# Kernel optimization log

Measured on AMD Instinct MI355X. Metric: run time of the kernel, lower is better.

The kernel has to match this reference:

```python
import jax, jax.numpy as jnp
import numpy as np

B, LV, HW, LT, D, H = 4, 16, 196, 32, 768, 12
DH = D // H
SCALE = 1.0 / np.sqrt(DH).astype(np.float32)


def _lin(x, W, b):
    # torch nn.Linear convention: W is [out, in]
    return x @ W.T + b


def _split_heads(x):
    # (..., D) -> (..., H, DH)
    return x.reshape(*x.shape[:-1], H, DH)


def _attn_logits(feat_q, feat_k, mask_q, mask_k, Wq, bq, Wk, bk):
    # feat_q: (B, LV, Lq, D), feat_k: (B, LV, Lk, D)
    q = _split_heads(_lin(feat_q, Wq, bq))  # b v q h d
    k = _split_heads(_lin(feat_k, Wk, bk))  # b v k h d
    logits = jnp.einsum('bvqhd,bvkhd->bvhqk', q, k)
    m = (mask_q[:, :, None] & mask_k[:, None, :])[:, None, None]  # b 1 1 q k
    return jnp.where(m, logits, -10000.0)


def setup_inputs() -> dict:
    key = jax.random.key(0)
    ks = jax.random.split(key, 12)
    inp = {
        'vid_feat': jax.random.normal(ks[0], (B, LV, HW, D), jnp.float32),
        'txt_feat': jax.random.normal(ks[1], (B, LV, LT, D), jnp.float32),
        'vid_mask': jnp.ones((B, LV), dtype=bool),
        'txt_mask': jax.random.randint(ks[2], (B, LT), 0, 2) > 0,
    }
    for i, name in enumerate(['v2v', 't2v', 't2t', 'v2t']):
        inp[name + '_W'] = jax.random.normal(ks[3 + 2 * i], (3, D, D), jnp.float32) * 0.02
        inp[name + '_b'] = jnp.zeros((3, D), jnp.float32)
    return inp


def reference(vid_feat, txt_feat, vid_mask, txt_mask,
              v2v_W, v2v_b, t2v_W, t2v_b, t2t_W, t2t_b, v2t_W, v2t_b):
    mask_hw = jnp.ones((vid_feat.shape[0], HW), dtype=bool)

    # values: concat video-keys then text-keys along the key axis
    v_value = jnp.concatenate([_lin(vid_feat, v2v_W[2], v2v_b[2]),
                               _lin(txt_feat, t2v_W[2], t2v_b[2])], axis=2)
    v_value = _split_heads(v_value)  # b v (HW+LT) h d
    t_value = jnp.concatenate([_lin(vid_feat, v2t_W[2], v2t_b[2]),
                               _lin(txt_feat, t2t_W[2], t2t_b[2])], axis=2)
    t_value = _split_heads(t_value)

    # logits (source call order: get_attn_logits(feat_k, mask_k, feat_q, mask_q, ...))
    v2v = _attn_logits(vid_feat, vid_feat, mask_hw, mask_hw, v2v_W[0], v2v_b[0], v2v_W[1], v2v_b[1])
    t2v = _attn_logits(vid_feat, txt_feat, mask_hw, txt_mask, t2v_W[0], t2v_b[0], t2v_W[1], t2v_b[1])
    v2t = _attn_logits(txt_feat, vid_feat, txt_mask, mask_hw, v2t_W[0], v2t_b[0], v2t_W[1], v2t_b[1])
    t2t = _attn_logits(txt_feat, txt_feat, txt_mask, txt_mask, t2t_W[0], t2t_b[0], t2t_W[1], t2t_b[1])

    v_logits = jnp.concatenate([v2v, t2v], axis=-1)  # b v h HW (HW+LT)
    t_logits = jnp.concatenate([v2t, t2t], axis=-1)  # b v h LT (HW+LT)

    # NOTE: source scales probabilities AFTER softmax by 1/sqrt(d_head)
    vid_out = jnp.einsum('bvhqk,bvkhd->bvqhd', jax.nn.softmax(v_logits, axis=-1) * SCALE, v_value)
    vid_out = vid_out.reshape(*vid_out.shape[:3], D)
    txt_out = jnp.einsum('bvhqk,bvkhd->bvqhd', jax.nn.softmax(t_logits, axis=-1) * SCALE, t_value)
    txt_out = txt_out.reshape(*txt_out.shape[:3], D)
    return (vid_out, txt_out)
```

## Files before the change

### kernel.cpp

```cpp
#include <hip/hip_runtime.h>

#define NBV 64
#define HWN 196
#define LTN 32
#define DIM 768
#define NH 12
#define DHD 64
#define ATT_SCALE 0.125f

typedef __attribute__((ext_vector_type(8))) __bf16 bf16x8;
typedef __attribute__((ext_vector_type(4))) float f32x4;

static __device__ __forceinline__ unsigned short f2bf(float f) {
    union { float f; unsigned u; } v; v.f = f;
    unsigned r = v.u + 0x7FFFu + ((v.u >> 16) & 1u);
    return (unsigned short)(r >> 16);
}

#define MFMA16(a, b, c) __builtin_amdgcn_mfma_f32_16x16x32_bf16((a), (b), (c), 0, 0, 0)
#define GLOAD_LDS16(g, l)                                                      \
    __builtin_amdgcn_global_load_lds(                                          \
        (const __attribute__((address_space(1))) void*)(g),                    \
        (__attribute__((address_space(3))) void*)(l), 16, 0, 0)

struct CvtCfg {
    const float* src[14];
    unsigned short* dst[14];
    int n4[14];
};

__global__ __launch_bounds__(256) void cvt_bf16(CvtCfg cfg) {
    const int e = blockIdx.y;
    const float4* s = (const float4*)cfg.src[e];
    unsigned short* d = cfg.dst[e];
    const int n4 = cfg.n4[e];
    for (int i = blockIdx.x * 256 + threadIdx.x; i < n4; i += gridDim.x * 256) {
        float4 v = s[i];
        ushort4 o;
        o.x = f2bf(v.x); o.y = f2bf(v.y); o.z = f2bf(v.z); o.w = f2bf(v.w);
        *(ushort4*)(d + (long)i * 4) = o;
    }
}

struct GemmCfg {
    const unsigned short* A[2];
    const unsigned short* W[2];
    unsigned short* out[2];
    const float* bias[2][6];
    int M[2];
};

__global__ __launch_bounds__(512, 2) void gemm_proj(GemmCfg cfg, int nb0)
{
    __shared__ __align__(16) unsigned short lds[36864];
    const int tid = threadIdx.x;
    const int lane = tid & 63, wid = tid >> 6;
    const int wm = wid >> 2, wn = wid & 3;
    const int fr = lane & 15, fg = lane >> 4;

    const int nwg = gridDim.x;
    const int orig = blockIdx.x;
    const int q = nwg >> 3, r = nwg & 7;
    const int xcd = orig & 7, lid = orig >> 3;
    const int wg = (xcd < r ? xcd * (q + 1) : r * (q + 1) + (xcd - r) * q) + lid;

    const int set = wg >= nb0;
    const int local = wg - (set ? nb0 : 0);
    const int mt = local / 18, nt = local - mt * 18;
    const int m0 = mt * 256, n0 = nt * 256;
    const int M = cfg.M[set];
    const unsigned short* __restrict__ A = cfg.A[set];
    const unsigned short* __restrict__ W = cfg.W[set];

    const int srow = tid >> 2;
    const int sxor = ((tid & 3) ^ ((tid >> 3) & 3)) * 8;
    const unsigned short* aSrc = A + (long)(m0 + srow) * DIM + sxor;
    const unsigned short* bSrc = W + (long)(n0 + srow) * DIM + sxor;
    unsigned short* ldst = lds + tid * 8;

    const int rxor = (fg ^ ((fr >> 1) & 3)) * 8;
    const int aoff = (wm * 128 + fr) * 32 + rxor;
    const int boff = 8192 + (wn * 64 + fr) * 32 + rxor;

    f32x4 acc[8][4] = {};

#define STAGE(t, s) do {                                                       \
    const unsigned short* _a = aSrc + (t) * 32;                                \
    const unsigned short* _b = bSrc + (t) * 32;                                \
    unsigned short* _d = ldst + (s) * 16384;                                   \
    GLOAD_LDS16(_a, _d);                                                       \
    GLOAD_LDS16(_a + 98304, _d + 4096);                                        \
    GLOAD_LDS16(_b, _d + 8192);                                                \
    GLOAD_LDS16(_b + 98304, _d + 12288);                                       \
} while (0)

#define WAITVM(n) asm volatile("s_waitcnt vmcnt(" #n ")" ::: "memory")

#define COMPUTE(s) do {                                                        \
    const unsigned short* _sa = lds + (s) * 16384 + aoff;                      \
    const unsigned short* _sb = lds + (s) * 16384 + boff;                      \
    bf16x8 af[8], bg[4];                                                       \
    _Pragma("unroll") for (int m = 0; m < 4; ++m)                              \
        af[m] = *(const bf16x8*)(_sa + m * 512);                               \
    _Pragma("unroll") for (int n = 0; n < 4; ++n)                              \
        bg[n] = *(const bf16x8*)(_sb + n * 512);                               \
    _Pragma("unroll") for (int m = 4; m < 8; ++m)                              \
        af[m] = *(const bf16x8*)(_sa + m * 512);                               \
    __builtin_amdgcn_s_setprio(1);                                             \
    _Pragma("unroll") for (int m = 0; m < 4; ++m)                              \
    _Pragma("unroll") for (int n = 0; n < 4; ++n)                              \
        acc[m][n] = MFMA16(bg[n], af[m], acc[m][n]);                           \
    __builtin_amdgcn_s_setprio(0);                                             \
    __builtin_amdgcn_s_setprio(1);                                             \
    _Pragma("unroll") for (int m = 4; m < 8; ++m)                              \
    _Pragma("unroll") for (int n = 0; n < 4; ++n)                              \
        acc[m][n] = MFMA16(bg[n], af[m], acc[m][n]);                           \
    __builtin_amdgcn_s_setprio(0);                                             \
} while (0)

    STAGE(0, 0);
#pragma unroll 1
    for (int t = 0; t < 23; ++t) {
        STAGE(t + 1, (t + 1) & 1);
        WAITVM(4);
        __builtin_amdgcn_s_barrier();
        COMPUTE(t & 1);
        asm volatile("" ::: "memory");
        __builtin_amdgcn_s_barrier();
    }
    WAITVM(0);
    __builtin_amdgcn_s_barrier();
    COMPUTE(1);

#undef COMPUTE
#undef WAITVM
#undef STAGE

    const int w = nt / 3;
    const int nlb = (nt - w * 3) * 256;
    const float* bp = cfg.bias[set][w];
    unsigned short* op = cfg.out[set] + (long)w * M * DIM;
    const int colL = wn * 64;
    asm volatile("" ::: "memory");
    __builtin_amdgcn_s_barrier();
#pragma unroll
    for (int p = 0; p < 2; ++p) {
        if (wm == p) {
#pragma unroll
            for (int n = 0; n < 4; ++n) {
                float4 b4 = *(const float4*)(bp + nlb + colL + n * 16 + fg * 4);
#pragma unroll
                for (int m = 0; m < 8; ++m) {
                    ushort4 u;
                    u.x = f2bf(acc[m][n][0] + b4.x);
                    u.y = f2bf(acc[m][n][1] + b4.y);
                    u.z = f2bf(acc[m][n][2] + b4.z);
                    u.w = f2bf(acc[m][n][3] + b4.w);
                    *(ushort4*)&lds[(m * 16 + fr) * 264 + colL + n * 16 + fg * 4] = u;
                }
            }
        }
        __builtin_amdgcn_s_barrier();
#pragma unroll
        for (int i = 0; i < 8; ++i) {
            int chunk = tid + i * 512;
            int rr = chunk >> 5, cb = chunk & 31;
            bf16x8 v = *(const bf16x8*)&lds[rr * 264 + cb * 8];
            *(bf16x8*)(op + (long)(m0 + p * 128 + rr) * DIM + nlb + cb * 8) = v;
        }
        if (p == 0) __builtin_amdgcn_s_barrier();
    }
}

struct TransCfg {
    const unsigned short* src[4];
    unsigned short* dst[4];
};

__global__ __launch_bounds__(256) void transpose_v(TransCfg cfg)
{
    __shared__ unsigned short t[32][33];
    const int x = blockIdx.x;
    const int which = x >> 3;
    const int xi = x & 7;
    const int istxt = (xi == 7);
    const unsigned short* src = cfg.src[which * 2 + istxt];
    unsigned short* dst = cfg.dst[which];
    const int nrows = istxt ? LTN : HWN;
    const int colbase = istxt ? 208 : 0;
    const int rt = istxt ? 0 : xi;

    const int bv = blockIdx.z, dt = blockIdx.y;
    const int tx = threadIdx.x & 31, ty = threadIdx.x >> 5;
#pragma unroll
    for (int i = 0; i < 4; ++i) {
        int r = rt * 32 + ty + i * 8;
        t[ty + i * 8][tx] = (r < nrows)
            ? src[(long)(bv * nrows + r) * DIM + dt * 32 + tx] : (unsigned short)0;
    }
    __syncthreads();
#pragma unroll
    for (int i = 0; i < 4; ++i) {
        int d = dt * 32 + ty + i * 8;
        int rr = rt * 32 + tx;
        if (rr < nrows)
            dst[(long)(bv * DIM + d) * 256 + colbase + rr] = t[tx][ty + i * 8];
    }
}

struct AttnCfg {
    const unsigned short* QA[2];
    const unsigned short* QB[2];
    const unsigned short* KV[2];
    const unsigned short* KT[2];
    const unsigned short* Vt[2];
    float* outp[2];
};

__global__ __launch_bounds__(256, 2) void attn_kernel(AttnCfg cfg,
                                                      const int* __restrict__ tmask)
{
    __shared__ __align__(16) unsigned short P[4][16][264];
    const int tid = threadIdx.x, lane = tid & 63, wid = tid >> 6;
    const int bv = blockIdx.x, h = blockIdx.y;
    const int b = bv >> 4;
    const int sel = (blockIdx.z == 4);
    const int nq = sel ? LTN : HWN;
    const unsigned short* QA = cfg.QA[sel];
    const unsigned short* QB = cfg.QB[sel];
    const unsigned short* KV = cfg.KV[sel];
    const unsigned short* KT = cfg.KT[sel];
    const unsigned short* Vt = cfg.Vt[sel];
    float* outp = cfg.outp[sel];
    const int q0 = (sel ? 0 : blockIdx.z * 64) + wid * 16;
    const int fr = lane & 15, fg = lane >> 4;

    int qr = q0 + fr; if (qr > nq - 1) qr = nq - 1;
    const unsigned short* qa_p = QA + (long)(bv * nq + qr) * DIM + h * DHD;
    const unsigned short* qb_p = QB + (long)(bv * nq + qr) * DIM + h * DHD;
    bf16x8 qa[2], qb[2];
#pragma unroll
    for (int kh = 0; kh < 2; ++kh) {
        qa[kh] = *(const bf16x8*)(qa_p + kh * 32 + fg * 8);
        qb[kh] = *(const bf16x8*)(qb_p + kh * 32 + fg * 8);
    }

    f32x4 acc[15];
#pragma unroll
    for (int kb = 0; kb < 13; ++kb) {
        int kr = kb * 16 + fr; if (kr > HWN - 1) kr = HWN - 1;
        const unsigned short* kp = KV + (long)(bv * HWN + kr) * DIM + h * DHD;
        f32x4 c = {0.f, 0.f, 0.f, 0.f};
        c = MFMA16(*(const bf16x8*)(kp + fg * 8), qa[0], c);
        c = MFMA16(*(const bf16x8*)(kp + 32 + fg * 8), qa[1], c);
        acc[kb] = c;
    }
#pragma unroll
    for (int kb = 13; kb < 15; ++kb) {
        int kr = (kb - 13) * 16 + fr;
        const unsigned short* kp = KT + (long)(bv * LTN + kr) * DIM + h * DHD;
        f32x4 c = {0.f, 0.f, 0.f, 0.f};
        c = MFMA16(*(const bf16x8*)(kp + fg * 8), qb[0], c);
        c = MFMA16(*(const bf16x8*)(kp + 32 + fg * 8), qb[1], c);
        acc[kb] = c;
    }

    int tm = tmask[b * LTN + (lane & 31)];
    bool vq = true;
    if (sel) {
        int qi = q0 + fr; if (qi > LTN - 1) qi = LTN - 1;
        vq = __shfl(tm, qi, 64) != 0;
    }
#pragma unroll
    for (int kb = 0; kb < 15; ++kb) {
#pragma unroll
        for (int j = 0; j < 4; ++j) {
            int c = kb * 16 + fg * 4 + j;
            bool kreal = (c < HWN) || (c >= 208);
            bool kvalid = true;
            if (c >= 208) kvalid = __shfl(tm, c - 208, 64) != 0;
            float l = acc[kb][j];
            if (!kreal) l = -3.0e38f;
            else if (!(kvalid && vq)) l = -10000.0f;
            acc[kb][j] = l;
        }
    }

    float mx = -3.0e38f;
#pragma unroll
    for (int kb = 0; kb < 15; ++kb)
#pragma unroll
        for (int j = 0; j < 4; ++j) mx = fmaxf(mx, acc[kb][j]);
    mx = fmaxf(mx, __shfl_xor(mx, 16, 64));
    mx = fmaxf(mx, __shfl_xor(mx, 32, 64));
    float s = 0.f;
#pragma unroll
    for (int kb = 0; kb < 15; ++kb)
#pragma unroll
        for (int j = 0; j < 4; ++j) {
            float p = __expf(acc[kb][j] - mx);
            acc[kb][j] = p;
            s += p;
        }
    s += __shfl_xor(s, 16, 64);
    s += __shfl_xor(s, 32, 64);

    unsigned short* pw = &P[wid][fr][0];
#pragma unroll
    for (int kb = 0; kb < 15; ++kb) {
        ushort4 u;
        u.x = f2bf(acc[kb][0]); u.y = f2bf(acc[kb][1]);
        u.z = f2bf(acc[kb][2]); u.w = f2bf(acc[kb][3]);
        *(ushort4*)(pw + kb * 16 + fg * 4) = u;
    }
    {
        ushort4 z = {0, 0, 0, 0};
        *(ushort4*)(pw + 240 + fg * 4) = z;
    }

    f32x4 oacc[4] = {};
    const unsigned short* vt_base = Vt + ((long)bv * DIM + h * DHD) * 256;
#pragma unroll
    for (int ks = 0; ks < 8; ++ks) {
        bf16x8 pf = *(const bf16x8*)(pw + ks * 32 + fg * 8);
#pragma unroll
        for (int n = 0; n < 4; ++n) {
            const unsigned short* vp = vt_base + (long)(n * 16 + fr) * 256 + ks * 32 + fg * 8;
            oacc[n] = MFMA16(*(const bf16x8*)vp, pf, oacc[n]);
        }
    }

    if (q0 + fr < nq) {
        float inv = ATT_SCALE / s;
        float* ob = outp + (long)(bv * nq + q0 + fr) * DIM + h * DHD;
#pragma unroll
        for (int n = 0; n < 4; ++n) {
            float4 o;
            o.x = oacc[n][0] * inv; o.y = oacc[n][1] * inv;
            o.z = oacc[n][2] * inv; o.w = oacc[n][3] * inv;
            *(float4*)(ob + n * 16 + fg * 4) = o;
        }
    }
}

extern "C" void kernel_launch(void* const* d_in, const int* in_sizes, int n_in,
                              void* d_out, int out_size, void* d_ws, size_t ws_size,
                              hipStream_t stream)
{
    const float* vid_feat = (const float*)d_in[0];
    const float* txt_feat = (const float*)d_in[1];
    const int*   txt_mask = (const int*)d_in[3];
    const float* v2v_W = (const float*)d_in[4];
    const float* v2v_b = (const float*)d_in[5];
    const float* t2v_W = (const float*)d_in[6];
    const float* t2v_b = (const float*)d_in[7];
    const float* t2t_W = (const float*)d_in[8];
    const float* t2t_b = (const float*)d_in[9];
    const float* v2t_W = (const float*)d_in[10];
    const float* v2t_b = (const float*)d_in[11];

    char* ws = (char*)d_ws;
    unsigned short* vid_bf   = (unsigned short*)(ws);
    unsigned short* txt_bf   = (unsigned short*)(ws + 19267584L);
    unsigned short* Wv_bf    = (unsigned short*)(ws + 22413312L);
    unsigned short* Wt_bf    = (unsigned short*)(ws + 29491200L);
    unsigned short* proj_vid = (unsigned short*)(ws + 36569088L);
    unsigned short* proj_txt = (unsigned short*)(ws + 152174592L);
    unsigned short* Vt_v     = (unsigned short*)(ws + 171048960L);
    unsigned short* Vt_t     = (unsigned short*)(ws + 196214784L);

    const long WSL = 589824;
    CvtCfg cc;
    cc.src[0] = vid_feat; cc.dst[0] = vid_bf; cc.n4[0] = 9633792 / 4;
    cc.src[1] = txt_feat; cc.dst[1] = txt_bf; cc.n4[1] = 1572864 / 4;
    const float* wsrc_v[6] = { v2v_W, v2v_W + WSL, t2v_W, v2t_W + WSL,
                               v2v_W + 2 * WSL, v2t_W + 2 * WSL };
    const float* wsrc_t[6] = { t2v_W + WSL, t2v_W + 2 * WSL, v2t_W, t2t_W,
                               t2t_W + WSL, t2t_W + 2 * WSL };
    for (int i = 0; i < 6; ++i) {
        cc.src[2 + i] = wsrc_v[i]; cc.dst[2 + i] = Wv_bf + (long)i * WSL; cc.n4[2 + i] = WSL / 4;
        cc.src[8 + i] = wsrc_t[i]; cc.dst[8 + i] = Wt_bf + (long)i * WSL; cc.n4[8 + i] = WSL / 4;
    }
    cvt_bf16<<<dim3(2048, 14), 256, 0, stream>>>(cc);

    GemmCfg gc;
    gc.A[0] = vid_bf;  gc.W[0] = Wv_bf;  gc.out[0] = proj_vid;  gc.M[0] = 12544;
    gc.A[1] = txt_bf;  gc.W[1] = Wt_bf;  gc.out[1] = proj_txt;  gc.M[1] = 2048;
    const float* bsrc_v[6] = { v2v_b, v2v_b + 768, t2v_b, v2t_b + 768,
                               v2v_b + 1536, v2t_b + 1536 };
    const float* bsrc_t[6] = { t2v_b + 768, t2v_b + 1536, v2t_b, t2t_b,
                               t2t_b + 768, t2t_b + 1536 };
    for (int i = 0; i < 6; ++i) { gc.bias[0][i] = bsrc_v[i]; gc.bias[1][i] = bsrc_t[i]; }
    gemm_proj<<<dim3(49 * 18 + 8 * 18), 512, 0, stream>>>(gc, 49 * 18);

    const long PV = 12544L * 768, PT = 2048L * 768;
    TransCfg tc;
    tc.src[0] = proj_vid + 4 * PV;  tc.src[1] = proj_txt + 1 * PT;  tc.dst[0] = Vt_v;
    tc.src[2] = proj_vid + 5 * PV;  tc.src[3] = proj_txt + 5 * PT;  tc.dst[1] = Vt_t;
    transpose_v<<<dim3(16, 24, 64), 256, 0, stream>>>(tc);

    float* out_f = (float*)d_out;
    AttnCfg ac;
    ac.QA[0] = proj_vid + 0 * PV;  ac.QB[0] = proj_vid + 2 * PV;
    ac.KV[0] = proj_vid + 1 * PV;  ac.KT[0] = proj_txt + 0 * PT;
    ac.Vt[0] = Vt_v;               ac.outp[0] = out_f;
    ac.QA[1] = proj_txt + 2 * PT;  ac.QB[1] = proj_txt + 3 * PT;
    ac.KV[1] = proj_vid + 3 * PV;  ac.KT[1] = proj_txt + 4 * PT;
    ac.Vt[1] = Vt_t;               ac.outp[1] = out_f + 9633792;
    attn_kernel<<<dim3(64, 12, 5), 256, 0, stream>>>(ac, txt_mask);
}
```

Before: 293.2 us.

## Deepen GEMM LDS pipeline to four stages with interleaved MFMA scheduling

The projection GEMM moves from a two-stage to a four-stage LDS ring buffer with three tiles prefetched. Each iteration now uses one barrier instead of two. The compute loop loads A fragments in pairs interleaved with MFMAs instead of preloading all eight, and sched_group_barrier hints interleave LDS reads, global-to-LDS loads and MFMAs, aiming to hide memory latency and cut register pressure. LDS grows to 128 KB per block, which may limit the two-blocks-per-CU occupancy the launch bounds request.

```diff
diff --git a/kernel.cpp b/kernel.cpp
--- a/kernel.cpp
+++ b/kernel.cpp
@@ -22,6 +22,7 @@
     __builtin_amdgcn_global_load_lds(                                          \
         (const __attribute__((address_space(1))) void*)(g),                    \
         (__attribute__((address_space(3))) void*)(l), 16, 0, 0)
+#define SGB __builtin_amdgcn_sched_group_barrier
 
 struct CvtCfg {
     const float* src[14];
@@ -52,7 +53,7 @@
 
 __global__ __launch_bounds__(512, 2) void gemm_proj(GemmCfg cfg, int nb0)
 {
-    __shared__ __align__(16) unsigned short lds[36864];
+    __shared__ __align__(16) unsigned short lds[65536];
     const int tid = threadIdx.x;
     const int lane = tid & 63, wid = tid >> 6;
     const int wm = wid >> 2, wn = wid & 3;
@@ -94,46 +95,72 @@
     GLOAD_LDS16(_b + 98304, _d + 12288);                                       \
 } while (0)
 
-#define WAITVM(n) asm volatile("s_waitcnt vmcnt(" #n ")" ::: "memory")
+#define MQUAD(mi, a) do {                                                      \
+    __builtin_amdgcn_s_setprio(1);                                             \
+    acc[mi][0] = MFMA16(bg0, a, acc[mi][0]);                                   \
+    acc[mi][1] = MFMA16(bg1, a, acc[mi][1]);                                   \
+    acc[mi][2] = MFMA16(bg2, a, acc[mi][2]);                                   \
+    acc[mi][3] = MFMA16(bg3, a, acc[mi][3]);                                   \
+    __builtin_amdgcn_s_setprio(0);                                             \
+} while (0)
 
 #define COMPUTE(s) do {                                                        \
     const unsigned short* _sa = lds + (s) * 16384 + aoff;                      \
     const unsigned short* _sb = lds + (s) * 16384 + boff;                      \
-    bf16x8 af[8], bg[4];                                                       \
-    _Pragma("unroll") for (int m = 0; m < 4; ++m)                              \
-        af[m] = *(const bf16x8*)(_sa + m * 512);                               \
-    _Pragma("unroll") for (int n = 0; n < 4; ++n)                              \
-        bg[n] = *(const bf16x8*)(_sb + n * 512);                               \
-    _Pragma("unroll") for (int m = 4; m < 8; ++m)                              \
-        af[m] = *(const bf16x8*)(_sa + m * 512);                               \
-    __builtin_amdgcn_s_setprio(1);                                             \
-    _Pragma("unroll") for (int m = 0; m < 4; ++m)                              \
-    _Pragma("unroll") for (int n = 0; n < 4; ++n)                              \
-        acc[m][n] = MFMA16(bg[n], af[m], acc[m][n]);                           \
-    __builtin_amdgcn_s_setprio(0);                                             \
-    __builtin_amdgcn_s_setprio(1);                                             \
-    _Pragma("unroll") for (int m = 4; m < 8; ++m)                              \
-    _Pragma("unroll") for (int n = 0; n < 4; ++n)                              \
-        acc[m][n] = MFMA16(bg[n], af[m], acc[m][n]);                           \
-    __builtin_amdgcn_s_setprio(0);                                             \
+    bf16x8 a0, a1, bg0, bg1, bg2, bg3;                                         \
+    bg0 = *(const bf16x8*)(_sb);        bg1 = *(const bf16x8*)(_sb + 512);     \
+    bg2 = *(const bf16x8*)(_sb + 1024); bg3 = *(const bf16x8*)(_sb + 1536);    \
+    a0 = *(const bf16x8*)(_sa);         a1 = *(const bf16x8*)(_sa + 512);      \
+    MQUAD(0, a0); MQUAD(1, a1);                                                \
+    a0 = *(const bf16x8*)(_sa + 1024);  a1 = *(const bf16x8*)(_sa + 1536);     \
+    MQUAD(2, a0); MQUAD(3, a1);                                                \
+    a0 = *(const bf16x8*)(_sa + 2048);  a1 = *(const bf16x8*)(_sa + 2560);     \
+    MQUAD(4, a0); MQUAD(5, a1);                                                \
+    a0 = *(const bf16x8*)(_sa + 3072);  a1 = *(const bf16x8*)(_sa + 3584);     \
+    MQUAD(6, a0); MQUAD(7, a1);                                                \
 } while (0)
 
-    STAGE(0, 0);
+#define SGB_CHAIN_S do {                                                       \
+    SGB(0x20, 4, 0);                                                           \
+    SGB(0x100, 6, 0); SGB(0x8, 8, 0);                                          \
+    SGB(0x100, 2, 0); SGB(0x8, 8, 0);                                          \
+    SGB(0x100, 2, 0); SGB(0x8, 8, 0);                                          \
+    SGB(0x100, 2, 0); SGB(0x8, 8, 0);                                          \
+} while (0)
+
+#define SGB_CHAIN_N do {                                                       \
+    SGB(0x100, 6, 0); SGB(0x8, 8, 0);                                          \
+    SGB(0x100, 2, 0); SGB(0x8, 8, 0);                                          \
+    SGB(0x100, 2, 0); SGB(0x8, 8, 0);                                          \
+    SGB(0x100, 2, 0); SGB(0x8, 8, 0);                                          \
+} while (0)
+
+#define WAITVM(n) asm volatile("s_waitcnt vmcnt(" #n ")" ::: "memory")
+
+    STAGE(0, 0); STAGE(1, 1); STAGE(2, 2);
 #pragma unroll 1
-    for (int t = 0; t < 23; ++t) {
-        STAGE(t + 1, (t + 1) & 1);
-        WAITVM(4);
+    for (int t = 0; t < 21; ++t) {
+        WAITVM(8);
         __builtin_amdgcn_s_barrier();
-        COMPUTE(t & 1);
-        asm volatile("" ::: "memory");
-        __builtin_amdgcn_s_barrier();
-    }
+        STAGE(t + 3, (t + 3) & 3);
+        COMPUTE(t & 3);
+        SGB_CHAIN_S;
+    }
+    WAITVM(8);
+    __builtin_amdgcn_s_barrier();
+    COMPUTE(1); SGB_CHAIN_N;
+    WAITVM(4);
+    __builtin_amdgcn_s_barrier();
+    COMPUTE(2); SGB_CHAIN_N;
     WAITVM(0);
     __builtin_amdgcn_s_barrier();
-    COMPUTE(1);
-
+    COMPUTE(3); SGB_CHAIN_N;
+
+#undef WAITVM
+#undef SGB_CHAIN_N
+#undef SGB_CHAIN_S
 #undef COMPUTE
-#undef WAITVM
+#undef MQUAD
 #undef STAGE
 
     const int w = nt / 3;
```

Measured after the change: 295.3 us. No clear change (+0.7%).

## Shrink projection GEMM tiles to 128x128 with triple-buffered LDS pipeline

Applied to the files above, without the earlier changes.

The projection GEMM moves from 256x256 tiles on 512-thread blocks with double buffering to 128x128 tiles on 256-thread blocks with three LDS stages. The loop now needs only one barrier per K step, and the launch bound allows three blocks per CU. The aim is more blocks for load balancing, smaller wave-quantization tails and better latency hiding. The trade-off is less data reuse per tile, so more global and L2 traffic for A and W.

```diff
diff --git a/kernel.cpp b/kernel.cpp
--- a/kernel.cpp
+++ b/kernel.cpp
@@ -50,12 +50,12 @@
     int M[2];
 };
 
-__global__ __launch_bounds__(512, 2) void gemm_proj(GemmCfg cfg, int nb0)
+__global__ __launch_bounds__(256, 3) void gemm_proj(GemmCfg cfg, int nb0)
 {
-    __shared__ __align__(16) unsigned short lds[36864];
+    __shared__ __align__(16) unsigned short lds[24576];
     const int tid = threadIdx.x;
     const int lane = tid & 63, wid = tid >> 6;
-    const int wm = wid >> 2, wn = wid & 3;
+    const int wm = wid >> 1, wn = wid & 1;
     const int fr = lane & 15, fg = lane >> 4;
 
     const int nwg = gridDim.x;
@@ -66,8 +66,8 @@
 
     const int set = wg >= nb0;
     const int local = wg - (set ? nb0 : 0);
-    const int mt = local / 18, nt = local - mt * 18;
-    const int m0 = mt * 256, n0 = nt * 256;
+    const int mt = local / 36, nt = local - mt * 36;
+    const int m0 = mt * 128, n0 = nt * 128;
     const int M = cfg.M[set];
     const unsigned short* __restrict__ A = cfg.A[set];
     const unsigned short* __restrict__ W = cfg.W[set];
@@ -79,96 +79,89 @@
     unsigned short* ldst = lds + tid * 8;
 
     const int rxor = (fg ^ ((fr >> 1) & 3)) * 8;
-    const int aoff = (wm * 128 + fr) * 32 + rxor;
-    const int boff = 8192 + (wn * 64 + fr) * 32 + rxor;
-
-    f32x4 acc[8][4] = {};
+    const int aoff = fr * 32 + rxor;
+    const int boff = 4096 + (wn * 64 + fr) * 32 + rxor;
+
+    f32x4 acc[4][4] = {};
 
 #define STAGE(t, s) do {                                                       \
     const unsigned short* _a = aSrc + (t) * 32;                                \
     const unsigned short* _b = bSrc + (t) * 32;                                \
-    unsigned short* _d = ldst + (s) * 16384;                                   \
+    unsigned short* _d = ldst + (s) * 8192;                                    \
     GLOAD_LDS16(_a, _d);                                                       \
-    GLOAD_LDS16(_a + 98304, _d + 4096);                                        \
-    GLOAD_LDS16(_b, _d + 8192);                                                \
-    GLOAD_LDS16(_b + 98304, _d + 12288);                                       \
+    GLOAD_LDS16(_a + 49152, _d + 2048);                                        \
+    GLOAD_LDS16(_b, _d + 4096);                                                \
+    GLOAD_LDS16(_b + 49152, _d + 6144);                                        \
 } while (0)
 
 #define WAITVM(n) asm volatile("s_waitcnt vmcnt(" #n ")" ::: "memory")
 
 #define COMPUTE(s) do {                                                        \
-    const unsigned short* _sa = lds + (s) * 16384 + aoff;                      \
-    const unsigned short* _sb = lds + (s) * 16384 + boff;                      \
-    bf16x8 af[8], bg[4];                                                       \
+    const unsigned short* _sa = lds + (s) * 8192 + (wm * 64) * 32 + aoff;      \
+    const unsigned short* _sb = lds + (s) * 8192 + boff;                       \
+    bf16x8 af[4], bg[4];                                                       \
     _Pragma("unroll") for (int m = 0; m < 4; ++m)                              \
         af[m] = *(const bf16x8*)(_sa + m * 512);                               \
     _Pragma("unroll") for (int n = 0; n < 4; ++n)                              \
         bg[n] = *(const bf16x8*)(_sb + n * 512);                               \
-    _Pragma("unroll") for (int m = 4; m < 8; ++m)                              \
-        af[m] = *(const bf16x8*)(_sa + m * 512);                               \
     __builtin_amdgcn_s_setprio(1);                                             \
     _Pragma("unroll") for (int m = 0; m < 4; ++m)                              \
     _Pragma("unroll") for (int n = 0; n < 4; ++n)                              \
         acc[m][n] = MFMA16(bg[n], af[m], acc[m][n]);                           \
     __builtin_amdgcn_s_setprio(0);                                             \
-    __builtin_amdgcn_s_setprio(1);                                             \
-    _Pragma("unroll") for (int m = 4; m < 8; ++m)                              \
-    _Pragma("unroll") for (int n = 0; n < 4; ++n)                              \
-        acc[m][n] = MFMA16(bg[n], af[m], acc[m][n]);                           \
-    __builtin_amdgcn_s_setprio(0);                                             \
 } while (0)
 
-    STAGE(0, 0);
+    STAGE(0, 0); STAGE(1, 1);
+    {
+        int s0 = 0, s2 = 2;
 #pragma unroll 1
-    for (int t = 0; t < 23; ++t) {
-        STAGE(t + 1, (t + 1) & 1);
+        for (int t = 0; t < 22; ++t) {
+            WAITVM(4);
+            __builtin_amdgcn_s_barrier();
+            STAGE(t + 2, s2);
+            COMPUTE(s0);
+            s0 = s0 == 2 ? 0 : s0 + 1;
+            s2 = s2 == 2 ? 0 : s2 + 1;
+        }
         WAITVM(4);
         __builtin_amdgcn_s_barrier();
-        COMPUTE(t & 1);
-        asm volatile("" ::: "memory");
+        COMPUTE(s0);
+        s0 = s0 == 2 ? 0 : s0 + 1;
+        WAITVM(0);
         __builtin_amdgcn_s_barrier();
-    }
-    WAITVM(0);
-    __builtin_amdgcn_s_barrier();
-    COMPUTE(1);
+        COMPUTE(s0);
+    }
 
 #undef COMPUTE
 #undef WAITVM
 #undef STAGE
 
-    const int w = nt / 3;
-    const int nlb = (nt - w * 3) * 256;
+    const int w = nt / 6;
+    const int nlb = (nt - w * 6) * 128;
     const float* bp = cfg.bias[set][w];
     unsigned short* op = cfg.out[set] + (long)w * M * DIM;
-    const int colL = wn * 64;
     asm volatile("" ::: "memory");
     __builtin_amdgcn_s_barrier();
 #pragma unroll
-    for (int p = 0; p < 2; ++p) {
-        if (wm == p) {
-#pragma unroll
-            for (int n = 0; n < 4; ++n) {
-                float4 b4 = *(const float4*)(bp + nlb + colL + n * 16 + fg * 4);
-#pragma unroll
-                for (int m = 0; m < 8; ++m) {
-                    ushort4 u;
-                    u.x = f2bf(acc[m][n][0] + b4.x);
-                    u.y = f2bf(acc[m][n][1] + b4.y);
-                    u.z = f2bf(acc[m][n][2] + b4.z);
-                    u.w = f2bf(acc[m][n][3] + b4.w);
-                    *(ushort4*)&lds[(m * 16 + fr) * 264 + colL + n * 16 + fg * 4] = u;
-                }
-            }
-        }
-        __builtin_amdgcn_s_barrier();
-#pragma unroll
-        for (int i = 0; i < 8; ++i) {
-            int chunk = tid + i * 512;
-            int rr = chunk >> 5, cb = chunk & 31;
-            bf16x8 v = *(const bf16x8*)&lds[rr * 264 + cb * 8];
-            *(bf16x8*)(op + (long)(m0 + p * 128 + rr) * DIM + nlb + cb * 8) = v;
-        }
-        if (p == 0) __builtin_amdgcn_s_barrier();
+    for (int n = 0; n < 4; ++n) {
+        float4 b4 = *(const float4*)(bp + nlb + wn * 64 + n * 16 + fg * 4);
+#pragma unroll
+        for (int m = 0; m < 4; ++m) {
+            ushort4 u;
+            u.x = f2bf(acc[m][n][0] + b4.x);
+            u.y = f2bf(acc[m][n][1] + b4.y);
+            u.z = f2bf(acc[m][n][2] + b4.z);
+            u.w = f2bf(acc[m][n][3] + b4.w);
+            *(ushort4*)&lds[(wm * 64 + m * 16 + fr) * 132 + wn * 64 + n * 16 + fg * 4] = u;
+        }
+    }
+    __builtin_amdgcn_s_barrier();
+#pragma unroll
+    for (int i = 0; i < 8; ++i) {
+        int chunk = tid + i * 256;
+        int rr = chunk >> 4, cb = chunk & 15;
+        bf16x8 v = *(const bf16x8*)&lds[rr * 132 + cb * 8];
+        *(bf16x8*)(op + (long)(m0 + rr) * DIM + nlb + cb * 8) = v;
     }
 }
 
@@ -391,7 +384,7 @@
     const float* bsrc_t[6] = { t2v_b + 768, t2v_b + 1536, v2t_b, t2t_b,
                                t2t_b + 768, t2t_b + 1536 };
     for (int i = 0; i < 6; ++i) { gc.bias[0][i] = bsrc_v[i]; gc.bias[1][i] = bsrc_t[i]; }
-    gemm_proj<<<dim3(49 * 18 + 8 * 18), 512, 0, stream>>>(gc, 49 * 18);
+    gemm_proj<<<dim3(98 * 36 + 16 * 36), 256, 0, stream>>>(gc, 98 * 36);
 
     const long PV = 12544L * 768, PT = 2048L * 768;
     TransCfg tc;
```

Measured after the change: 304.9 us. +4.0%, slower.
